# Optimization experiments

Measured on AMD Instinct MI355X. Metric: run time of the kernel, lower is better.

## Reference

```python
import jax, jax.numpy as jnp
import numpy as np

N_NODES = 100000
N_EDGES = 1600000
IN_F = 64
HIDDEN = 128
HIDDEN2 = HIDDEN // 2
N_CLASSES = 10


def setup_inputs() -> dict:
    key = jax.random.key(0)
    ks = jax.random.split(key, 8)
    x = jax.random.normal(ks[0], (N_NODES, IN_F), dtype=jnp.float32)
    edge_index = jax.random.randint(ks[1], (2, N_EDGES), 0, N_NODES, dtype=jnp.int64 if jax.config.jax_enable_x64 else jnp.int32)
    # Linear params (PyTorch nn.Linear: y = x @ W.T + b); store as [in, out] for einsum-free matmul
    def lin(k, fi, fo):
        bound = 1.0 / np.sqrt(fi)
        kw, kb = jax.random.split(k)
        W = jax.random.uniform(kw, (fi, fo), minval=-bound, maxval=bound, dtype=jnp.float32)
        b = jax.random.uniform(kb, (fo,), minval=-bound, maxval=bound, dtype=jnp.float32)
        return W, b
    W1, b1 = lin(ks[2], IN_F, HIDDEN)
    W2, b2 = lin(ks[3], HIDDEN, HIDDEN2)
    W3, b3 = lin(ks[4], HIDDEN2, N_CLASSES)
    return {"x": x, "edge_index": edge_index, "n_nodes": N_NODES,
            "W1": W1, "b1": b1, "W2": W2, "b2": b2, "W3": W3, "b3": b3}


def gcn_layer(x, row, col, n_nodes, W, b):
    # gather source features, scatter-add into destination nodes
    agg = jax.ops.segment_sum(x[row], col, num_segments=n_nodes)  # [N, F]
    deg = jax.ops.segment_sum(jnp.ones_like(col, dtype=x.dtype), col, num_segments=n_nodes)
    deg = jnp.maximum(deg, 1.0)
    return (agg / deg[:, None]) @ W + b


def reference(x, edge_index, n_nodes, W1, b1, W2, b2, W3, b3):
    row, col = edge_index[0], edge_index[1]
    h = jax.nn.relu(gcn_layer(x, row, col, n_nodes, W1, b1))
    # dropout is identity in eval mode
    h = jax.nn.relu(gcn_layer(h, row, col, n_nodes, W2, b2))
    return h @ W3 + b3
```

## Files before the change

### kernel.cpp

```cpp
#include <hip/hip_runtime.h>

#define N_NODES 100000
#define N_EDGES 1600000
#define IN_F 64
#define HID 128
#define HID2 64
#define NCLS 10

#define SEG 64

#define NBUCK 128
#define SUBR 782
#define CAP2 14000
#define EBA 6250

typedef __attribute__((ext_vector_type(8))) short bfrag;
typedef __attribute__((ext_vector_type(4))) float f32x4;

__device__ __forceinline__ unsigned short bf_rne(float f) {
  unsigned int u = __float_as_uint(f);
  u += 0x7fffu + ((u >> 16) & 1u);
  return (unsigned short)(u >> 16);
}

__global__ __launch_bounds__(256) void cast_k(const float* __restrict__ x,
                                              unsigned short* __restrict__ xb) {
  int i = blockIdx.x * blockDim.x + threadIdx.x;
  const float4* xf4 = (const float4*)x;
  float4 a = xf4[2 * i];
  float4 b = xf4[2 * i + 1];
  ushort4 o0, o1;
  o0.x = bf_rne(a.x); o0.y = bf_rne(a.y); o0.z = bf_rne(a.z); o0.w = bf_rne(a.w);
  o1.x = bf_rne(b.x); o1.y = bf_rne(b.y); o1.z = bf_rne(b.z); o1.w = bf_rne(b.w);
  ushort4* ob = (ushort4*)xb;
  ob[2 * i] = o0;
  ob[2 * i + 1] = o1;
}

__global__ __launch_bounds__(256) void wtrans_k(const float* __restrict__ W1,
                                                const float* __restrict__ W2,
                                                unsigned short* __restrict__ W1t,
                                                unsigned short* __restrict__ W2t) {
  int i = blockIdx.x * 256 + threadIdx.x;
  if (i < IN_F * HID) {
    int j = i >> 6, k = i & 63;
    W1t[i] = bf_rne(W1[k * HID + j]);
  } else {
    int i2 = i - IN_F * HID;
    int j = i2 >> 7, k = i2 & 127;
    W2t[i2] = bf_rne(W2[k * HID2 + j]);
  }
}

__global__ __launch_bounds__(256) void binA_k(const int* __restrict__ row,
                                              const int* __restrict__ col,
                                              int* __restrict__ bcnt,
                                              int2* __restrict__ pairs) {
  __shared__ int hcnt[NBUCK];
  __shared__ int hbase[NBUCK];
  int t = threadIdx.x;
  if (t < NBUCK) hcnt[t] = 0;
  __syncthreads();
  int e0 = blockIdx.x * EBA;
  int e1 = e0 + EBA;
  for (int e = e0 + t; e < e1; e += 256) {
    int b = col[e] / SUBR;
    atomicAdd(&hcnt[b], 1);
  }
  __syncthreads();
  if (t < NBUCK) {
    hbase[t] = atomicAdd(&bcnt[t], hcnt[t]);
    hcnt[t] = 0;
  }
  __syncthreads();
  for (int e = e0 + t; e < e1; e += 256) {
    int dst = col[e];
    int src = row[e];
    int b = dst / SUBR;
    int pos = hbase[b] + atomicAdd(&hcnt[b], 1);
    pairs[(size_t)b * CAP2 + pos] = make_int2(dst, src);
  }
}

__global__ __launch_bounds__(512) void binB_k(const int2* __restrict__ pairs,
                                              const int* __restrict__ bcnt,
                                              int* __restrict__ cursors,
                                              int* __restrict__ csr_src) {
  __shared__ int cur[SUBR];
  int b = blockIdx.x;
  int t = threadIdx.x;
  int lo = b * SUBR;
  for (int i = t; i < SUBR; i += 512) cur[i] = 0;
  __syncthreads();
  int cnt = bcnt[b];
  const int2* bp = pairs + (size_t)b * CAP2;
  for (int i = t; i < cnt; i += 512) {
    int2 p = bp[i];
    int pos = atomicAdd(&cur[p.x - lo], 1);
    csr_src[(size_t)p.x * SEG + pos] = p.y;
  }
  __syncthreads();
  for (int i = t; i < SUBR; i += 512) {
    int n = lo + i;
    if (n < N_NODES) {
      int d = cur[i];
      cursors[n] = n * SEG + d;
      int dp = (d + 15) & ~15;
      for (int q = d; q < dp; q++) csr_src[(size_t)n * SEG + q] = 0;
    }
  }
}

__device__ __forceinline__ float4 gather_bf16(const uint2* __restrict__ vb,
                                              const int* __restrict__ csr,
                                              int s, int e2, int padc,
                                              int eg, int fc) {
  float ax = 0.f, ay = 0.f, az = 0.f, aw = 0.f;
  const int4* csr4 = (const int4*)csr;
#define ACCUM(w)                                                    \
  {                                                                 \
    ax += __uint_as_float((w).x << 16);                             \
    ay += __uint_as_float((w).x & 0xffff0000u);                     \
    az += __uint_as_float((w).y << 16);                             \
    aw += __uint_as_float((w).y & 0xffff0000u);                     \
  }
  int p = s;
  for (; p + 32 <= e2; p += 32) {
    int4 iA = csr4[(p >> 2) + eg];
    int4 iB = csr4[((p + 16) >> 2) + eg];
    uint2 a0 = vb[(size_t)iA.x * 16 + fc];
    uint2 a1 = vb[(size_t)iA.y * 16 + fc];
    uint2 a2 = vb[(size_t)iA.z * 16 + fc];
    uint2 a3 = vb[(size_t)iA.w * 16 + fc];
    uint2 b0 = vb[(size_t)iB.x * 16 + fc];
    uint2 b1 = vb[(size_t)iB.y * 16 + fc];
    uint2 b2 = vb[(size_t)iB.z * 16 + fc];
    uint2 b3 = vb[(size_t)iB.w * 16 + fc];
    ACCUM(a0) ACCUM(a1) ACCUM(a2) ACCUM(a3)
    ACCUM(b0) ACCUM(b1) ACCUM(b2) ACCUM(b3)
  }
  if (p < e2) {
    int4 iA = csr4[(p >> 2) + eg];
    uint2 a0 = vb[(size_t)iA.x * 16 + fc];
    uint2 a1 = vb[(size_t)iA.y * 16 + fc];
    uint2 a2 = vb[(size_t)iA.z * 16 + fc];
    uint2 a3 = vb[(size_t)iA.w * 16 + fc];
    ACCUM(a0) ACCUM(a1) ACCUM(a2) ACCUM(a3)
  }
#undef ACCUM
  ax += __shfl_xor(ax, 16); ay += __shfl_xor(ay, 16);
  az += __shfl_xor(az, 16); aw += __shfl_xor(aw, 16);
  ax += __shfl_xor(ax, 32); ay += __shfl_xor(ay, 32);
  az += __shfl_xor(az, 32); aw += __shfl_xor(aw, 32);
  uint2 z = vb[fc];
  float pc = (float)padc;
  ax -= pc * __uint_as_float(z.x << 16);
  ay -= pc * __uint_as_float(z.x & 0xffff0000u);
  az -= pc * __uint_as_float(z.y << 16);
  aw -= pc * __uint_as_float(z.y & 0xffff0000u);
  return make_float4(ax, ay, az, aw);
}

#define NB1 32
#define XS_S 72
#define HS_S 136
#define W1_S 72
#define W2_S 136
__global__ __launch_bounds__(512) void gmm1_k(
    const unsigned short* __restrict__ xb, const int* __restrict__ cursors,
    const int* __restrict__ csr_src, const unsigned short* __restrict__ W1t,
    const float* __restrict__ b1, const unsigned short* __restrict__ W2t,
    unsigned short* __restrict__ g) {
  __shared__ unsigned short W1l[HID * W1_S];
  __shared__ unsigned short W2l[HID2 * W2_S];
  __shared__ unsigned short xsb[NB1 * XS_S];
  __shared__ unsigned short hsb[NB1 * HS_S];
  __shared__ float b1l[HID];
  int t = threadIdx.x;
  {
    const uint2* s1 = (const uint2*)W1t;
    for (int i = t; i < HID * IN_F / 4; i += 512) {
      int j = i >> 4, k4 = i & 15;
      *(uint2*)&W1l[j * W1_S + k4 * 4] = s1[i];
    }
    const uint2* s2 = (const uint2*)W2t;
    for (int i = t; i < HID2 * HID / 4; i += 512) {
      int j = i >> 5, k4 = i & 31;
      *(uint2*)&W2l[j * W2_S + k4 * 4] = s2[i];
    }
    if (t < HID) b1l[t] = b1[t];
  }
  int node0 = blockIdx.x * NB1;
  int wave = t >> 6;
  int lane = t & 63;
  int eg = lane >> 4;
  int fc = lane & 15;
  {
    const uint2* xv = (const uint2*)xb;
    for (int i = 0; i < 4; i++) {
      int ln = wave * 4 + i;
      int n = node0 + ln;
      int s = n * SEG;
      int d = cursors[n] - s;
      int dp = (d + 15) & ~15;
      float4 a = gather_bf16(xv, csr_src, s, s + dp, dp - d, eg, fc);
      float inv = 1.0f / (d < 1 ? 1.0f : (float)d);
      if (eg == 0) {
        ushort4 o;
        o.x = bf_rne(a.x * inv); o.y = bf_rne(a.y * inv);
        o.z = bf_rne(a.z * inv); o.w = bf_rne(a.w * inv);
        *(ushort4*)&xsb[ln * XS_S + fc * 4] = o;
      }
    }
  }
  __syncthreads();
  int lr = lane & 15;
  int kb = lane >> 4;
  {
    int c = wave;
#pragma unroll
    for (int m = 0; m < 2; m++) {
      f32x4 acc = {0.f, 0.f, 0.f, 0.f};
#pragma unroll
      for (int s = 0; s < 2; s++) {
        bfrag af = *(const bfrag*)&xsb[(m * 16 + lr) * XS_S + s * 32 + kb * 8];
        bfrag bf = *(const bfrag*)&W1l[(c * 16 + lr) * W1_S + s * 32 + kb * 8];
        acc = __builtin_amdgcn_mfma_f32_16x16x32_bf16(af, bf, acc, 0, 0, 0);
      }
      int col = c * 16 + lr;
      float bb = b1l[col];
#pragma unroll
      for (int q = 0; q < 4; q++) {
        int r = m * 16 + kb * 4 + q;
        float v = acc[q] + bb;
        hsb[r * HS_S + col] = bf_rne(v > 0.0f ? v : 0.0f);
      }
    }
  }
  __syncthreads();
  {
    int m = wave >> 2, c = wave & 3;
    f32x4 acc = {0.f, 0.f, 0.f, 0.f};
#pragma unroll
    for (int s = 0; s < 4; s++) {
      bfrag af = *(const bfrag*)&hsb[(m * 16 + lr) * HS_S + s * 32 + kb * 8];
      bfrag bf = *(const bfrag*)&W2l[(c * 16 + lr) * W2_S + s * 32 + kb * 8];
      acc = __builtin_amdgcn_mfma_f32_16x16x32_bf16(af, bf, acc, 0, 0, 0);
    }
    int col = c * 16 + lr;
#pragma unroll
    for (int q = 0; q < 4; q++) {
      int r = m * 16 + kb * 4 + q;
      g[(size_t)(node0 + r) * HID2 + col] = bf_rne(acc[q]);
    }
  }
}

#define NBH 32
__global__ __launch_bounds__(512) void ghead_k(
    const unsigned short* __restrict__ g, const int* __restrict__ cursors,
    const int* __restrict__ csr_src, const float* __restrict__ b2,
    const float* __restrict__ W3, const float* __restrict__ b3,
    float* __restrict__ out) {
  __shared__ float W3l[HID2 * NCLS];
  __shared__ float hs[NBH][HID2 + 4];
  int t = threadIdx.x;
  for (int i = t; i < HID2 * NCLS; i += 512) W3l[i] = W3[i];
  int node0 = blockIdx.x * NBH;
  int lane = t & 63;
  int wave = t >> 6;
  int eg = lane >> 4;
  int fc = lane & 15;
  const uint2* gv = (const uint2*)g;
  const float4* b2f4 = (const float4*)b2;
  for (int i = 0; i < 4; i++) {
    int ln = wave * 4 + i;
    int n = node0 + ln;
    int s = n * SEG;
    int d = cursors[n] - s;
    int dp = (d + 15) & ~15;
    float4 a = gather_bf16(gv, csr_src, s, s + dp, dp - d, eg, fc);
    float inv = 1.0f / (d < 1 ? 1.0f : (float)d);
    if (eg == 0) {
      float4 bb = b2f4[fc];
      float4 v;
      v.x = a.x * inv + bb.x; v.y = a.y * inv + bb.y;
      v.z = a.z * inv + bb.z; v.w = a.w * inv + bb.w;
      v.x = v.x > 0.0f ? v.x : 0.0f;
      v.y = v.y > 0.0f ? v.y : 0.0f;
      v.z = v.z > 0.0f ? v.z : 0.0f;
      v.w = v.w > 0.0f ? v.w : 0.0f;
      *(float4*)&hs[ln][fc * 4] = v;
    }
  }
  __syncthreads();
  if (t < NBH * NCLS) {
    int n = t / NCLS;
    int c = t - n * NCLS;
    float a = b3[c];
    for (int k = 0; k < HID2; k++) a += hs[n][k] * W3l[k * NCLS + c];
    out[(size_t)(node0 + n) * NCLS + c] = a;
  }
}

extern "C" void kernel_launch(void* const* d_in, const int* in_sizes, int n_in,
                              void* d_out, int out_size, void* d_ws, size_t ws_size,
                              hipStream_t stream) {
  const float* x  = (const float*)d_in[0];
  const int*   ei = (const int*)d_in[1];
  const int*   row = ei;
  const int*   col = ei + N_EDGES;
  const float* W1 = (const float*)d_in[3];
  const float* b1 = (const float*)d_in[4];
  const float* W2 = (const float*)d_in[5];
  const float* b2 = (const float*)d_in[6];
  const float* W3 = (const float*)d_in[7];
  const float* b3 = (const float*)d_in[8];
  float* out = (float*)d_out;

  char* ws = (char*)d_ws;
  int*            cursors = (int*)ws;
  int*            bcnt    = (int*)(ws + (512 << 10));
  unsigned short* W1t     = (unsigned short*)(ws + (520 << 10));
  unsigned short* W2t     = (unsigned short*)(ws + (552 << 10));
  int*            csr_src = (int*)(ws + (1 << 20));
  int2*           pairs   = (int2*)(ws + (28 << 20));
  unsigned short* xb      = (unsigned short*)(ws + (43 << 20));
  unsigned short* g       = (unsigned short*)(ws + (57 << 20));

  hipMemsetAsync(bcnt, 0, NBUCK * sizeof(int), stream);
  wtrans_k<<<(IN_F * HID + HID * HID2) / 256, 256, 0, stream>>>(W1, W2, W1t, W2t);
  cast_k<<<N_NODES * IN_F / 8 / 256, 256, 0, stream>>>(x, xb);
  binA_k<<<N_EDGES / EBA, 256, 0, stream>>>(row, col, bcnt, pairs);
  binB_k<<<NBUCK, 512, 0, stream>>>(pairs, bcnt, cursors, csr_src);

  gmm1_k<<<N_NODES / NB1, 512, 0, stream>>>(xb, cursors, csr_src, W1t, b1, W2t, g);

  ghead_k<<<N_NODES / NBH, 512, 0, stream>>>(g, cursors, csr_src, b2, W3, b3, out);
}
```

Measured before the change: 149.5 us.

## Pack bin pairs into 32-bit words and batch four-node gathers for memory-level parallelism

Edge pairs are packed into one 32-bit word (local destination in the high bits, source in the low 17 bits), halving the binning scratch traffic. The per-node gather loop is replaced by a four-node routine that issues the index loads and the first 32 neighbour loads for several nodes up front, with padding to at least 32 slots, so more memory requests are in flight per wave. Launch bounds now request four blocks per CU, and node degree is clamped to SEG. The trade-offs are higher register pressure, extra padded loads for low-degree nodes, and dropping of any neighbours beyond 64.

Measured after the change: 148.3 us. About the same (-0.8%).

```diff
diff --git a/kernel.cpp b/kernel.cpp
--- a/kernel.cpp
+++ b/kernel.cpp
@@ -55,7 +55,7 @@
 __global__ __launch_bounds__(256) void binA_k(const int* __restrict__ row,
                                               const int* __restrict__ col,
                                               int* __restrict__ bcnt,
-                                              int2* __restrict__ pairs) {
+                                              unsigned int* __restrict__ pairs) {
   __shared__ int hcnt[NBUCK];
   __shared__ int hbase[NBUCK];
   int t = threadIdx.x;
@@ -78,11 +78,12 @@
     int src = row[e];
     int b = dst / SUBR;
     int pos = hbase[b] + atomicAdd(&hcnt[b], 1);
-    pairs[(size_t)b * CAP2 + pos] = make_int2(dst, src);
-  }
-}
-
-__global__ __launch_bounds__(512) void binB_k(const int2* __restrict__ pairs,
+    pairs[(size_t)b * CAP2 + pos] =
+        ((unsigned)(dst - b * SUBR) << 17) | (unsigned)src;
+  }
+}
+
+__global__ __launch_bounds__(512) void binB_k(const unsigned int* __restrict__ pairs,
                                               const int* __restrict__ bcnt,
                                               int* __restrict__ cursors,
                                               int* __restrict__ csr_src) {
@@ -93,72 +94,101 @@
   for (int i = t; i < SUBR; i += 512) cur[i] = 0;
   __syncthreads();
   int cnt = bcnt[b];
-  const int2* bp = pairs + (size_t)b * CAP2;
+  const unsigned int* bp = pairs + (size_t)b * CAP2;
   for (int i = t; i < cnt; i += 512) {
-    int2 p = bp[i];
-    int pos = atomicAdd(&cur[p.x - lo], 1);
-    csr_src[(size_t)p.x * SEG + pos] = p.y;
+    unsigned w = bp[i];
+    int local = w >> 17;
+    int src = (int)(w & 0x1ffffu);
+    int pos = atomicAdd(&cur[local], 1);
+    if (pos < SEG) csr_src[(size_t)(lo + local) * SEG + pos] = src;
   }
   __syncthreads();
   for (int i = t; i < SUBR; i += 512) {
     int n = lo + i;
     if (n < N_NODES) {
       int d = cur[i];
+      if (d > SEG) d = SEG;
       cursors[n] = n * SEG + d;
-      int dp = (d + 15) & ~15;
-      for (int q = d; q < dp; q++) csr_src[(size_t)n * SEG + q] = 0;
-    }
-  }
-}
-
-__device__ __forceinline__ float4 gather_bf16(const uint2* __restrict__ vb,
-                                              const int* __restrict__ csr,
-                                              int s, int e2, int padc,
-                                              int eg, int fc) {
-  float ax = 0.f, ay = 0.f, az = 0.f, aw = 0.f;
+      int cons = d <= 32 ? 32 : ((d + 15) & ~15);
+      for (int q = d; q < cons; q++) csr_src[(size_t)n * SEG + q] = 0;
+    }
+  }
+}
+
+#define ACC1(r)                                                     \
+  {                                                                 \
+    ax += __uint_as_float((r).x << 16);                             \
+    ay += __uint_as_float((r).x & 0xffff0000u);                     \
+    az += __uint_as_float((r).y << 16);                             \
+    aw += __uint_as_float((r).y & 0xffff0000u);                     \
+  }
+#define LD8(r, ia, ib)                                              \
+  {                                                                 \
+    r[0] = vb[(size_t)(unsigned)(ia).x * 16 + fc];                  \
+    r[1] = vb[(size_t)(unsigned)(ia).y * 16 + fc];                  \
+    r[2] = vb[(size_t)(unsigned)(ia).z * 16 + fc];                  \
+    r[3] = vb[(size_t)(unsigned)(ia).w * 16 + fc];                  \
+    r[4] = vb[(size_t)(unsigned)(ib).x * 16 + fc];                  \
+    r[5] = vb[(size_t)(unsigned)(ib).y * 16 + fc];                  \
+    r[6] = vb[(size_t)(unsigned)(ib).z * 16 + fc];                  \
+    r[7] = vb[(size_t)(unsigned)(ib).w * 16 + fc];                  \
+  }
+#define NODE_BODY(i, rbuf, dd, EXTRA)                               \
+  {                                                                 \
+    float ax = 0.f, ay = 0.f, az = 0.f, aw = 0.f;                   \
+    ACC1(rbuf[0]) ACC1(rbuf[1]) ACC1(rbuf[2]) ACC1(rbuf[3])         \
+    ACC1(rbuf[4]) ACC1(rbuf[5]) ACC1(rbuf[6]) ACC1(rbuf[7])         \
+    int cons = 32;                                                  \
+    if (dd > 32) {                                                  \
+      cons = (dd + 15) & ~15;                                       \
+      int sbase = (n0 + i) * SEG;                                   \
+      for (int p = sbase + 32; p < sbase + cons; p += 16) {         \
+        int4 iT = csr4[(p >> 2) + eg];                              \
+        uint2 t0 = vb[(size_t)(unsigned)iT.x * 16 + fc];            \
+        uint2 t1 = vb[(size_t)(unsigned)iT.y * 16 + fc];            \
+        uint2 t2 = vb[(size_t)(unsigned)iT.z * 16 + fc];            \
+        uint2 t3 = vb[(size_t)(unsigned)iT.w * 16 + fc];            \
+        ACC1(t0) ACC1(t1) ACC1(t2) ACC1(t3)                         \
+      }                                                             \
+    }                                                               \
+    EXTRA                                                           \
+    ax += __shfl_xor(ax, 16); ay += __shfl_xor(ay, 16);             \
+    az += __shfl_xor(az, 16); aw += __shfl_xor(aw, 16);             \
+    ax += __shfl_xor(ax, 32); ay += __shfl_xor(ay, 32);             \
+    az += __shfl_xor(az, 32); aw += __shfl_xor(aw, 32);             \
+    float pc = (float)(cons - dd);                                  \
+    res[i] = make_float4(ax - pc * zx, ay - pc * zy,                \
+                         az - pc * zz, aw - pc * zw);               \
+    inv[i] = 1.0f / (dd < 1 ? 1.0f : (float)(dd));                  \
+  }
+
+__device__ __forceinline__ void gather4_bf16(
+    const uint2* __restrict__ vb, const int* __restrict__ csr,
+    const int* __restrict__ cursors, int n0, int eg, int fc,
+    float4 res[4], float inv[4]) {
   const int4* csr4 = (const int4*)csr;
-#define ACCUM(w)                                                    \
-  {                                                                 \
-    ax += __uint_as_float((w).x << 16);                             \
-    ay += __uint_as_float((w).x & 0xffff0000u);                     \
-    az += __uint_as_float((w).y << 16);                             \
-    aw += __uint_as_float((w).y & 0xffff0000u);                     \
-  }
-  int p = s;
-  for (; p + 32 <= e2; p += 32) {
-    int4 iA = csr4[(p >> 2) + eg];
-    int4 iB = csr4[((p + 16) >> 2) + eg];
-    uint2 a0 = vb[(size_t)iA.x * 16 + fc];
-    uint2 a1 = vb[(size_t)iA.y * 16 + fc];
-    uint2 a2 = vb[(size_t)iA.z * 16 + fc];
-    uint2 a3 = vb[(size_t)iA.w * 16 + fc];
-    uint2 b0 = vb[(size_t)iB.x * 16 + fc];
-    uint2 b1 = vb[(size_t)iB.y * 16 + fc];
-    uint2 b2 = vb[(size_t)iB.z * 16 + fc];
-    uint2 b3 = vb[(size_t)iB.w * 16 + fc];
-    ACCUM(a0) ACCUM(a1) ACCUM(a2) ACCUM(a3)
-    ACCUM(b0) ACCUM(b1) ACCUM(b2) ACCUM(b3)
-  }
-  if (p < e2) {
-    int4 iA = csr4[(p >> 2) + eg];
-    uint2 a0 = vb[(size_t)iA.x * 16 + fc];
-    uint2 a1 = vb[(size_t)iA.y * 16 + fc];
-    uint2 a2 = vb[(size_t)iA.z * 16 + fc];
-    uint2 a3 = vb[(size_t)iA.w * 16 + fc];
-    ACCUM(a0) ACCUM(a1) ACCUM(a2) ACCUM(a3)
-  }
-#undef ACCUM
-  ax += __shfl_xor(ax, 16); ay += __shfl_xor(ay, 16);
-  az += __shfl_xor(az, 16); aw += __shfl_xor(aw, 16);
-  ax += __shfl_xor(ax, 32); ay += __shfl_xor(ay, 32);
-  az += __shfl_xor(az, 32); aw += __shfl_xor(aw, 32);
+  size_t rb = (size_t)n0 * 16;
+  int4 iA0 = csr4[rb + eg],      iB0 = csr4[rb + 4 + eg];
+  int4 iA1 = csr4[rb + 16 + eg], iB1 = csr4[rb + 20 + eg];
+  int4 iA2 = csr4[rb + 32 + eg], iB2 = csr4[rb + 36 + eg];
+  int4 iA3 = csr4[rb + 48 + eg], iB3 = csr4[rb + 52 + eg];
+  int d0 = cursors[n0 + 0] - (n0 + 0) * SEG;
+  int d1 = cursors[n0 + 1] - (n0 + 1) * SEG;
+  int d2 = cursors[n0 + 2] - (n0 + 2) * SEG;
+  int d3 = cursors[n0 + 3] - (n0 + 3) * SEG;
+  uint2 rA[8], rB[8], rC[8];
+  LD8(rA, iA0, iB0)
+  LD8(rB, iA1, iB1)
+  LD8(rC, iA2, iB2)
   uint2 z = vb[fc];
-  float pc = (float)padc;
-  ax -= pc * __uint_as_float(z.x << 16);
-  ay -= pc * __uint_as_float(z.x & 0xffff0000u);
-  az -= pc * __uint_as_float(z.y << 16);
-  aw -= pc * __uint_as_float(z.y & 0xffff0000u);
-  return make_float4(ax, ay, az, aw);
+  float zx = __uint_as_float(z.x << 16);
+  float zy = __uint_as_float(z.x & 0xffff0000u);
+  float zz = __uint_as_float(z.y << 16);
+  float zw = __uint_as_float(z.y & 0xffff0000u);
+  NODE_BODY(0, rA, d0, LD8(rA, iA3, iB3))
+  NODE_BODY(1, rB, d1, )
+  NODE_BODY(2, rC, d2, )
+  NODE_BODY(3, rA, d3, )
 }
 
 #define NB1 32
@@ -166,7 +196,7 @@
 #define HS_S 136
 #define W1_S 72
 #define W2_S 136
-__global__ __launch_bounds__(512) void gmm1_k(
+__global__ __launch_bounds__(512, 4) void gmm1_k(
     const unsigned short* __restrict__ xb, const int* __restrict__ cursors,
     const int* __restrict__ csr_src, const unsigned short* __restrict__ W1t,
     const float* __restrict__ b1, const unsigned short* __restrict__ W2t,
@@ -196,20 +226,17 @@
   int eg = lane >> 4;
   int fc = lane & 15;
   {
-    const uint2* xv = (const uint2*)xb;
-    for (int i = 0; i < 4; i++) {
-      int ln = wave * 4 + i;
-      int n = node0 + ln;
-      int s = n * SEG;
-      int d = cursors[n] - s;
-      int dp = (d + 15) & ~15;
-      float4 a = gather_bf16(xv, csr_src, s, s + dp, dp - d, eg, fc);
-      float inv = 1.0f / (d < 1 ? 1.0f : (float)d);
-      if (eg == 0) {
+    const uint2* vb = (const uint2*)xb;
+    float4 res[4];
+    float inv[4];
+    gather4_bf16(vb, csr_src, cursors, node0 + wave * 4, eg, fc, res, inv);
+    if (eg == 0) {
+#pragma unroll
+      for (int i = 0; i < 4; i++) {
         ushort4 o;
-        o.x = bf_rne(a.x * inv); o.y = bf_rne(a.y * inv);
-        o.z = bf_rne(a.z * inv); o.w = bf_rne(a.w * inv);
-        *(ushort4*)&xsb[ln * XS_S + fc * 4] = o;
+        o.x = bf_rne(res[i].x * inv[i]); o.y = bf_rne(res[i].y * inv[i]);
+        o.z = bf_rne(res[i].z * inv[i]); o.w = bf_rne(res[i].w * inv[i]);
+        *(ushort4*)&xsb[(wave * 4 + i) * XS_S + fc * 4] = o;
       }
     }
   }
@@ -257,7 +284,7 @@
 }
 
 #define NBH 32
-__global__ __launch_bounds__(512) void ghead_k(
+__global__ __launch_bounds__(512, 4) void ghead_k(
     const unsigned short* __restrict__ g, const int* __restrict__ cursors,
     const int* __restrict__ csr_src, const float* __restrict__ b2,
     const float* __restrict__ W3, const float* __restrict__ b3,
@@ -271,26 +298,25 @@
   int wave = t >> 6;
   int eg = lane >> 4;
   int fc = lane & 15;
-  const uint2* gv = (const uint2*)g;
-  const float4* b2f4 = (const float4*)b2;
-  for (int i = 0; i < 4; i++) {
-    int ln = wave * 4 + i;
-    int n = node0 + ln;
-    int s = n * SEG;
-    int d = cursors[n] - s;
-    int dp = (d + 15) & ~15;
-    float4 a = gather_bf16(gv, csr_src, s, s + dp, dp - d, eg, fc);
-    float inv = 1.0f / (d < 1 ? 1.0f : (float)d);
+  {
+    const uint2* vb = (const uint2*)g;
+    const float4* b2f4 = (const float4*)b2;
+    float4 res[4];
+    float inv[4];
+    gather4_bf16(vb, csr_src, cursors, node0 + wave * 4, eg, fc, res, inv);
     if (eg == 0) {
       float4 bb = b2f4[fc];
-      float4 v;
-      v.x = a.x * inv + bb.x; v.y = a.y * inv + bb.y;
-      v.z = a.z * inv + bb.z; v.w = a.w * inv + bb.w;
-      v.x = v.x > 0.0f ? v.x : 0.0f;
-      v.y = v.y > 0.0f ? v.y : 0.0f;
-      v.z = v.z > 0.0f ? v.z : 0.0f;
-      v.w = v.w > 0.0f ? v.w : 0.0f;
-      *(float4*)&hs[ln][fc * 4] = v;
+#pragma unroll
+      for (int i = 0; i < 4; i++) {
+        float4 v;
+        v.x = res[i].x * inv[i] + bb.x; v.y = res[i].y * inv[i] + bb.y;
+        v.z = res[i].z * inv[i] + bb.z; v.w = res[i].w * inv[i] + bb.w;
+        v.x = v.x > 0.0f ? v.x : 0.0f;
+        v.y = v.y > 0.0f ? v.y : 0.0f;
+        v.z = v.z > 0.0f ? v.z : 0.0f;
+        v.w = v.w > 0.0f ? v.w : 0.0f;
+        *(float4*)&hs[wave * 4 + i][fc * 4] = v;
+      }
     }
   }
   __syncthreads();
@@ -324,9 +350,9 @@
   unsigned short* W1t     = (unsigned short*)(ws + (520 << 10));
   unsigned short* W2t     = (unsigned short*)(ws + (552 << 10));
   int*            csr_src = (int*)(ws + (1 << 20));
-  int2*           pairs   = (int2*)(ws + (28 << 20));
-  unsigned short* xb      = (unsigned short*)(ws + (43 << 20));
-  unsigned short* g       = (unsigned short*)(ws + (57 << 20));
+  unsigned int*   pairs   = (unsigned int*)(ws + (28 << 20));
+  unsigned short* xb      = (unsigned short*)(ws + (36 << 20));
+  unsigned short* g       = (unsigned short*)(ws + (49 << 20));
 
   hipMemsetAsync(bcnt, 0, NBUCK * sizeof(int), stream);
   wtrans_k<<<(IN_F * HID + HID * HID2) / 256, 256, 0, stream>>>(W1, W2, W1t, W2t);
```
